# Kernel tuning notes

Measured on AMD Instinct MI355X. Metric: run time of the kernel, lower is better.

The kernel has to match this reference:

```python
import jax, jax.numpy as jnp
import numpy as np

SCALE = 1.0
P0 = 0.1


def setup_inputs() -> dict:
    key = jax.random.key(0)
    k1, k2, k3, k4 = jax.random.split(key, 4)
    B, N, D, T, TM = 64, 2048, 128, 512, 512
    data = jax.random.normal(k1, (B, N, D), dtype=jnp.float32)
    targets = jax.random.normal(k2, (B, N), dtype=jnp.float32)
    W = jax.random.normal(k3, (D, T), dtype=jnp.float32)        # major task pool, (n_dims, n_tasks)
    W_minor = jax.random.normal(k4, (D, TM), dtype=jnp.float32)  # minor task pool
    return {"data": data, "targets": targets, "W": W, "W_minor": W_minor}


def reference(data, targets, W, W_minor):
    # data: (B, N, D); targets: (B, N); W: (D, T); W_minor: (D, TM)
    n_minor = W_minor.shape[1]
    W_all = jnp.concatenate([W, W_minor], axis=1)            # (D, T_total)
    XW = jnp.einsum('bnd,dt->bnt', data, W_all)              # (B, N, T_total)
    diff2 = (targets[..., None] - XW) ** 2                   # (B, N, T_total)
    # Prefix sum-of-squared-residuals: step i uses points 0..i-1 (step 0 -> zeros,
    # matching the original's zeros-prefix call).
    prefix = jnp.cumsum(diff2, axis=1)
    prefix = jnp.concatenate([jnp.zeros_like(prefix[:, :1]), prefix[:, :-1]], axis=1)
    # Log priors: original hardcodes log((1-p0)/3) for major tasks (kept faithfully).
    log_prior_major = float(np.log((1.0 - P0) / 3.0))
    log_prior_minor = float(np.log(P0 / n_minor))
    log_prior = jnp.concatenate([
        jnp.full((W.shape[1],), log_prior_major, dtype=data.dtype),
        jnp.full((n_minor,), log_prior_minor, dtype=data.dtype),
    ])                                                        # (T_total,)
    log_probs = -0.5 * prefix / (SCALE ** 2) + log_prior      # (B, N, T_total)
    weights = jax.nn.softmax(log_probs, axis=-1)              # posterior over tasks
    w_mmse = jnp.einsum('bnt,dt->bnd', weights, W_all)        # (B, N, D)
    preds = jnp.sum(data * w_mmse, axis=-1)                   # (B, N)
    return preds
```

## Files before the change

kernel.cpp:

```cpp
#include <hip/hip_runtime.h>

typedef _Float16 half8 __attribute__((ext_vector_type(8)));
typedef float floatx4 __attribute__((ext_vector_type(4)));

#define NB 64
#define NN 2048
#define ND 128
#define NT 1024
#define NC 16
#define NCHUNKS 128
#define NIV 64

#define ALPHA 0.84932184f
#define INV_ALPHA 1.17741002f
#define LP2_MAJOR (-1.7369655941662063f)
#define LP2_MINOR (-12.321928094887362f)

__device__ __forceinline__ float fexp2(float x) {
  float r;
  asm("v_exp_f32 %0, %1" : "=v"(r) : "v"(x));
  return r;
}

#define PIN8(x) asm volatile("" : "+v"(x))

template <int CTRL>
__device__ __forceinline__ float dppshr_add(float x) {
  int i = __builtin_bit_cast(int, x);
  int s = __builtin_amdgcn_update_dpp(0, i, CTRL, 0xF, 0xF, true);
  return x + __builtin_bit_cast(float, s);
}
__device__ __forceinline__ float scan16(float x) {
  x = dppshr_add<0x111>(x);
  x = dppshr_add<0x112>(x);
  x = dppshr_add<0x114>(x);
  x = dppshr_add<0x118>(x);
  return x;
}
__device__ __forceinline__ float bcast15(float x) {
  int i = __builtin_bit_cast(int, x);
  i = __builtin_amdgcn_ds_swizzle(i, 0x1F0);
  return __builtin_bit_cast(float, i);
}

__global__ void k_prep(const float* __restrict__ W, const float* __restrict__ Wm,
                       _Float16* __restrict__ Wph, _Float16* __restrict__ Wpl) {
  int idx = blockIdx.x * 256 + threadIdx.x;
  int t = idx >> 7, d = idx & 127;
  float x = (t < 512) ? W[d * 512 + t] : Wm[d * 512 + (t - 512)];
  x *= ALPHA;
  _Float16 h = (_Float16)x;
  _Float16 l = (_Float16)(x - (float)h);
  Wph[idx] = h;
  Wpl[idx] = l;
}

__global__ void k_prep_data(const float* __restrict__ data,
                            _Float16* __restrict__ Apk) {
  int idx = blockIdx.x * 256 + threadIdx.x;
  int l = idx & 63, kk = (idx >> 6) & 3, ch = (idx >> 8) & 127, b = idx >> 15;
  int row = ch * 16 + (l & 15);
  int dcol = kk * 32 + (l >> 4) * 8;
  const float* src = data + ((size_t)b * NN + row) * ND + dcol;
  floatx4 a0 = *(const floatx4*)src;
  floatx4 a1 = *(const floatx4*)(src + 4);
  half8 h, lo;
#pragma unroll
  for (int j = 0; j < 4; ++j) {
    h[j] = (_Float16)a0[j];
    lo[j] = (_Float16)(a0[j] - (float)h[j]);
    h[4 + j] = (_Float16)a1[j];
    lo[4 + j] = (_Float16)(a1[j] - (float)h[4 + j]);
  }
  size_t o = ((size_t)(b * 128 + ch)) * 4096 + kk * 512 + l * 8;
  *(half8*)(Apk + o) = h;
  *(half8*)(Apk + o + 2048) = lo;
}

__global__ __launch_bounds__(512, 4)
void k_fused(const _Float16* __restrict__ Apk, const float* __restrict__ targets,
             const _Float16* __restrict__ Wph, const _Float16* __restrict__ Wpl,
             floatx4* __restrict__ part) {
  int bid = blockIdx.x;
  int xcd = bid & 7, rest = bid >> 3;
  int tq = rest & 7, b = (rest >> 3) * 8 + xcd;
  int tid = threadIdx.x;
  int w = tid >> 6, l = tid & 63;
  int l15 = l & 15, lhi = l >> 4;
  int wavebase = tq * 128 + w * 16;

  half8 wh[4], wl[4];
#pragma unroll
  for (int kk = 0; kk < 4; ++kk) {
    int off = (wavebase + l15) * 128 + kk * 32 + lhi * 8;
    wh[kk] = *(const half8*)(Wph + off);
    wl[kk] = *(const half8*)(Wpl + off);
  }
#pragma unroll
  for (int kk = 0; kk < 4; ++kk) { PIN8(wh[kk]); PIN8(wl[kk]); }

  float prior2 = (tq < 4) ? LP2_MAJOR : LP2_MINOR;
  float run[4] = {0.f, 0.f, 0.f, 0.f};

  const _Float16* abase = Apk + (size_t)b * 128 * 4096;
  const float* tgp = targets + (size_t)b * NN + l15;
  size_t pbase = (size_t)b * NN * 8 + tq;

  __shared__ _Float16 Abuf[2][2][4096];
  __shared__ float sm[8][4][65][3];

  int wslot = w * 512 + l * 8;

#define EPI(ACC, SLOT, TGOFF)                                         \
  do {                                                                \
    float tgs = tgp[TGOFF] * ALPHA;                                   \
    float q[4], inc[4], lp[4];                                        \
    _Pragma("unroll")                                                 \
    for (int r = 0; r < 4; ++r) {                                     \
      float d = tgs - ACC[r];                                         \
      q[r] = d * d;                                                   \
    }                                                                 \
    _Pragma("unroll")                                                 \
    for (int r = 0; r < 4; ++r) inc[r] = scan16(q[r]);                \
    _Pragma("unroll")                                                 \
    for (int r = 0; r < 4; ++r)                                       \
      lp[r] = (prior2 - run[r]) + (q[r] - inc[r]);                    \
    _Pragma("unroll")                                                 \
    for (int r = 0; r < 4; ++r) run[r] += bcast15(inc[r]);            \
    float m = fmaxf(fmaxf(lp[0], lp[1]), fmaxf(lp[2], lp[3]));        \
    float s1 = 0.f, s2 = 0.f;                                         \
    _Pragma("unroll")                                                 \
    for (int r = 0; r < 4; ++r) {                                     \
      float e = fexp2(lp[r] - m);                                     \
      s1 += e;                                                        \
      s2 = fmaf(e, ACC[r], s2);                                       \
    }                                                                 \
    sm[w][SLOT][l][0] = m;                                            \
    sm[w][SLOT][l][1] = s1;                                           \
    sm[w][SLOT][l][2] = s2;                                           \
  } while (0)

#define GEMM3(ACC, AH, AL)                                                        \
  do {                                                                            \
    floatx4 hh = {0.f, 0.f, 0.f, 0.f};                                            \
    floatx4 hl = {0.f, 0.f, 0.f, 0.f};                                            \
    floatx4 lh = {0.f, 0.f, 0.f, 0.f};                                            \
    _Pragma("unroll")                                                             \
    for (int kk = 0; kk < 4; ++kk) {                                              \
      hh = __builtin_amdgcn_mfma_f32_16x16x32_f16(wh[kk], AH[kk], hh, 0, 0, 0);   \
      hl = __builtin_amdgcn_mfma_f32_16x16x32_f16(wh[kk], AL[kk], hl, 0, 0, 0);   \
      lh = __builtin_amdgcn_mfma_f32_16x16x32_f16(wl[kk], AH[kk], lh, 0, 0, 0);   \
    }                                                                             \
    ACC = (hh + hl) + lh;                                                         \
  } while (0)

  half8 s0 = *(const half8*)(abase + wslot);
  half8 s1 = *(const half8*)(abase + 4096 + wslot);
  *(half8*)&Abuf[0][0][wslot] = s0;
  *(half8*)&Abuf[0][1][wslot] = s1;
  s0 = *(const half8*)(abase + 2 * 4096 + wslot);
  s1 = *(const half8*)(abase + 3 * 4096 + wslot);
  __syncthreads();

  for (int iv = 0; iv < NIV; ++iv) {
    int cur = iv & 1;
    half8 ahA[4], alA[4];
#pragma unroll
    for (int kk = 0; kk < 4; ++kk) {
      ahA[kk] = *(const half8*)&Abuf[cur][0][kk * 512 + l * 8];
      alA[kk] = *(const half8*)&Abuf[cur][0][2048 + kk * 512 + l * 8];
    }
    floatx4 accA;
    GEMM3(accA, ahA, alA);
    half8 ahB[4], alB[4];
#pragma unroll
    for (int kk = 0; kk < 4; ++kk) {
      ahB[kk] = *(const half8*)&Abuf[cur][1][kk * 512 + l * 8];
      alB[kk] = *(const half8*)&Abuf[cur][1][2048 + kk * 512 + l * 8];
    }
    floatx4 accB;
    GEMM3(accB, ahB, alB);

    *(half8*)&Abuf[cur ^ 1][0][wslot] = s0;
    *(half8*)&Abuf[cur ^ 1][1][wslot] = s1;
    int pfA = 2 * iv + 4, pfB = 2 * iv + 5;
    pfA = pfA > 127 ? 127 : pfA;
    pfB = pfB > 127 ? 127 : pfB;
    s0 = *(const half8*)(abase + (size_t)pfA * 4096 + wslot);
    s1 = *(const half8*)(abase + (size_t)pfB * 4096 + wslot);

    EPI(accA, ((2 * iv) & 3), 0);
    EPI(accB, ((2 * iv + 1) & 3), 16);

    if (iv & 1) {
      __syncthreads();
      if (tid < 64) {
        int c4 = tid >> 4, row = tid & 15;
        float M = -3.4e38f;
#pragma unroll
        for (int wv = 0; wv < 8; ++wv)
#pragma unroll
          for (int g = 0; g < 4; ++g)
            M = fmaxf(M, sm[wv][c4][g * 16 + row][0]);
        float S1 = 0.f, S2 = 0.f;
#pragma unroll
        for (int wv = 0; wv < 8; ++wv)
#pragma unroll
          for (int g = 0; g < 4; ++g) {
            float e = fexp2(sm[wv][c4][g * 16 + row][0] - M);
            S1 = fmaf(sm[wv][c4][g * 16 + row][1], e, S1);
            S2 = fmaf(sm[wv][c4][g * 16 + row][2], e, S2);
          }
        floatx4 v;
        v[0] = M; v[1] = S1; v[2] = S2; v[3] = 0.f;
        part[pbase + (size_t)((2 * iv - 2 + c4) * 16 + row) * 8] = v;
      }
    }
    __syncthreads();
    tgp += 32;
  }
#undef EPI
#undef GEMM3
}

__global__ void k_combine(const floatx4* __restrict__ part, float* __restrict__ out) {
  int idx = blockIdx.x * 256 + threadIdx.x;
  const floatx4* p = part + (size_t)idx * 8;
  floatx4 v[8];
  float M = -3.4e38f;
#pragma unroll
  for (int j = 0; j < 8; ++j) { v[j] = p[j]; M = fmaxf(M, v[j][0]); }
  float s1 = 0.f, s2 = 0.f;
#pragma unroll
  for (int j = 0; j < 8; ++j) {
    float e = fexp2(v[j][0] - M);
    s1 += v[j][1] * e;
    s2 += v[j][2] * e;
  }
  out[idx] = s2 / s1 * INV_ALPHA;
}

extern "C" void kernel_launch(void* const* d_in, const int* in_sizes, int n_in,
                              void* d_out, int out_size, void* d_ws, size_t ws_size,
                              hipStream_t stream) {
  const float* data    = (const float*)d_in[0];
  const float* targets = (const float*)d_in[1];
  const float* W       = (const float*)d_in[2];
  const float* Wm      = (const float*)d_in[3];
  float* out = (float*)d_out;

  char* ws = (char*)d_ws;
  const size_t MB = 1u << 20;
  _Float16* Wph  = (_Float16*)ws;
  _Float16* Wpl  = (_Float16*)(ws + 256 * 1024);
  _Float16* Apk  = (_Float16*)(ws + 512 * 1024);
  floatx4* part  = (floatx4*)(ws + 512 * 1024 + 64 * MB);

  k_prep<<<512, 256, 0, stream>>>(W, Wm, Wph, Wpl);
  k_prep_data<<<8192, 256, 0, stream>>>(data, Apk);
  k_fused<<<NB * 8, 512, 0, stream>>>(Apk, targets, Wph, Wpl, part);
  k_combine<<<(NB * NN) / 256, 256, 0, stream>>>(part, out);
}
```

Measured before the change: 182.3 us.

## Give each wave two task tiles and halve block size in fused kernel

Each wave now holds two 16-task weight tiles in registers and reuses every A fragment loaded from LDS for both tiles, so each block runs 4 waves of 256 threads instead of 8. This halves the LDS reads of A per MFMA and halves the softmax partial-merge work across waves. The cost is double the register footprint for the weights and accumulators and fewer waves per block, which may lower occupancy and latency hiding.

```diff
diff --git a/kernel.cpp b/kernel.cpp
--- a/kernel.cpp
+++ b/kernel.cpp
@@ -77,7 +77,7 @@
   *(half8*)(Apk + o + 2048) = lo;
 }
 
-__global__ __launch_bounds__(512, 4)
+__global__ __launch_bounds__(256, 2)
 void k_fused(const _Float16* __restrict__ Apk, const float* __restrict__ targets,
              const _Float16* __restrict__ Wph, const _Float16* __restrict__ Wpl,
              floatx4* __restrict__ part) {
@@ -87,110 +87,134 @@
   int tid = threadIdx.x;
   int w = tid >> 6, l = tid & 63;
   int l15 = l & 15, lhi = l >> 4;
-  int wavebase = tq * 128 + w * 16;
-
-  half8 wh[4], wl[4];
-#pragma unroll
-  for (int kk = 0; kk < 4; ++kk) {
-    int off = (wavebase + l15) * 128 + kk * 32 + lhi * 8;
-    wh[kk] = *(const half8*)(Wph + off);
-    wl[kk] = *(const half8*)(Wpl + off);
-  }
-#pragma unroll
-  for (int kk = 0; kk < 4; ++kk) { PIN8(wh[kk]); PIN8(wl[kk]); }
+  int wavebase = tq * 128 + w * 32;
+
+  half8 wh[2][4], wl[2][4];
+#pragma unroll
+  for (int tt = 0; tt < 2; ++tt)
+#pragma unroll
+    for (int kk = 0; kk < 4; ++kk) {
+      int off = (wavebase + tt * 16 + l15) * 128 + kk * 32 + lhi * 8;
+      wh[tt][kk] = *(const half8*)(Wph + off);
+      wl[tt][kk] = *(const half8*)(Wpl + off);
+    }
+#pragma unroll
+  for (int tt = 0; tt < 2; ++tt)
+#pragma unroll
+    for (int kk = 0; kk < 4; ++kk) { PIN8(wh[tt][kk]); PIN8(wl[tt][kk]); }
 
   float prior2 = (tq < 4) ? LP2_MAJOR : LP2_MINOR;
-  float run[4] = {0.f, 0.f, 0.f, 0.f};
+  float run[2][4] = {{0.f, 0.f, 0.f, 0.f}, {0.f, 0.f, 0.f, 0.f}};
 
   const _Float16* abase = Apk + (size_t)b * 128 * 4096;
   const float* tgp = targets + (size_t)b * NN + l15;
   size_t pbase = (size_t)b * NN * 8 + tq;
 
-  __shared__ _Float16 Abuf[2][2][4096];
-  __shared__ float sm[8][4][65][3];
-
-  int wslot = w * 512 + l * 8;
-
-#define EPI(ACC, SLOT, TGOFF)                                         \
+  __shared__ _Float16 Abuf[2][8192];
+  __shared__ float sm[4][4][65][3];
+
+  int t8 = tid * 8;
+
+#define GEMM3(ACC, TT, AH, AL)                                                      \
+  do {                                                                              \
+    floatx4 hh = {0.f, 0.f, 0.f, 0.f};                                              \
+    floatx4 hl = {0.f, 0.f, 0.f, 0.f};                                              \
+    floatx4 lh = {0.f, 0.f, 0.f, 0.f};                                              \
+    _Pragma("unroll")                                                               \
+    for (int kk = 0; kk < 4; ++kk) {                                                \
+      hh = __builtin_amdgcn_mfma_f32_16x16x32_f16(wh[TT][kk], AH[kk], hh, 0, 0, 0); \
+      hl = __builtin_amdgcn_mfma_f32_16x16x32_f16(wh[TT][kk], AL[kk], hl, 0, 0, 0); \
+      lh = __builtin_amdgcn_mfma_f32_16x16x32_f16(wl[TT][kk], AH[kk], lh, 0, 0, 0); \
+    }                                                                               \
+    ACC = (hh + hl) + lh;                                                           \
+  } while (0)
+
+#define EPI(ACC0, ACC1, SLOT, TGOFF)                                  \
   do {                                                                \
     float tgs = tgp[TGOFF] * ALPHA;                                   \
-    float q[4], inc[4], lp[4];                                        \
+    float q[2][4], inc[2][4], lp[2][4];                               \
     _Pragma("unroll")                                                 \
     for (int r = 0; r < 4; ++r) {                                     \
-      float d = tgs - ACC[r];                                         \
-      q[r] = d * d;                                                   \
+      float d0 = tgs - ACC0[r], d1 = tgs - ACC1[r];                   \
+      q[0][r] = d0 * d0; q[1][r] = d1 * d1;                           \
     }                                                                 \
     _Pragma("unroll")                                                 \
-    for (int r = 0; r < 4; ++r) inc[r] = scan16(q[r]);                \
-    _Pragma("unroll")                                                 \
-    for (int r = 0; r < 4; ++r)                                       \
-      lp[r] = (prior2 - run[r]) + (q[r] - inc[r]);                    \
-    _Pragma("unroll")                                                 \
-    for (int r = 0; r < 4; ++r) run[r] += bcast15(inc[r]);            \
-    float m = fmaxf(fmaxf(lp[0], lp[1]), fmaxf(lp[2], lp[3]));        \
+    for (int tt = 0; tt < 2; ++tt)                                    \
+      _Pragma("unroll")                                               \
+      for (int r = 0; r < 4; ++r) inc[tt][r] = scan16(q[tt][r]);      \
+    _Pragma("unroll")                                                 \
+    for (int tt = 0; tt < 2; ++tt)                                    \
+      _Pragma("unroll")                                               \
+      for (int r = 0; r < 4; ++r) {                                   \
+        lp[tt][r] = (prior2 - run[tt][r]) + (q[tt][r] - inc[tt][r]);  \
+        run[tt][r] += bcast15(inc[tt][r]);                            \
+      }                                                               \
+    float m = fmaxf(fmaxf(fmaxf(lp[0][0], lp[0][1]),                  \
+                          fmaxf(lp[0][2], lp[0][3])),                 \
+                    fmaxf(fmaxf(lp[1][0], lp[1][1]),                  \
+                          fmaxf(lp[1][2], lp[1][3])));                \
     float s1 = 0.f, s2 = 0.f;                                         \
     _Pragma("unroll")                                                 \
     for (int r = 0; r < 4; ++r) {                                     \
-      float e = fexp2(lp[r] - m);                                     \
-      s1 += e;                                                        \
-      s2 = fmaf(e, ACC[r], s2);                                       \
+      float e0 = fexp2(lp[0][r] - m), e1 = fexp2(lp[1][r] - m);       \
+      s1 += e0 + e1;                                                  \
+      s2 = fmaf(e0, ACC0[r], s2);                                     \
+      s2 = fmaf(e1, ACC1[r], s2);                                     \
     }                                                                 \
     sm[w][SLOT][l][0] = m;                                            \
     sm[w][SLOT][l][1] = s1;                                           \
     sm[w][SLOT][l][2] = s2;                                           \
   } while (0)
 
-#define GEMM3(ACC, AH, AL)                                                        \
-  do {                                                                            \
-    floatx4 hh = {0.f, 0.f, 0.f, 0.f};                                            \
-    floatx4 hl = {0.f, 0.f, 0.f, 0.f};                                            \
-    floatx4 lh = {0.f, 0.f, 0.f, 0.f};                                            \
-    _Pragma("unroll")                                                             \
-    for (int kk = 0; kk < 4; ++kk) {                                              \
-      hh = __builtin_amdgcn_mfma_f32_16x16x32_f16(wh[kk], AH[kk], hh, 0, 0, 0);   \
-      hl = __builtin_amdgcn_mfma_f32_16x16x32_f16(wh[kk], AL[kk], hl, 0, 0, 0);   \
-      lh = __builtin_amdgcn_mfma_f32_16x16x32_f16(wl[kk], AH[kk], lh, 0, 0, 0);   \
-    }                                                                             \
-    ACC = (hh + hl) + lh;                                                         \
-  } while (0)
-
-  half8 s0 = *(const half8*)(abase + wslot);
-  half8 s1 = *(const half8*)(abase + 4096 + wslot);
-  *(half8*)&Abuf[0][0][wslot] = s0;
-  *(half8*)&Abuf[0][1][wslot] = s1;
-  s0 = *(const half8*)(abase + 2 * 4096 + wslot);
-  s1 = *(const half8*)(abase + 3 * 4096 + wslot);
+  half8 s0 = *(const half8*)(abase + t8);
+  half8 s1_ = *(const half8*)(abase + 2048 + t8);
+  half8 s2_ = *(const half8*)(abase + 4096 + t8);
+  half8 s3 = *(const half8*)(abase + 6144 + t8);
+  *(half8*)&Abuf[0][t8] = s0;
+  *(half8*)&Abuf[0][2048 + t8] = s1_;
+  *(half8*)&Abuf[0][4096 + t8] = s2_;
+  *(half8*)&Abuf[0][6144 + t8] = s3;
+  s0 = *(const half8*)(abase + 8192 + t8);
+  s1_ = *(const half8*)(abase + 8192 + 2048 + t8);
+  s2_ = *(const half8*)(abase + 8192 + 4096 + t8);
+  s3 = *(const half8*)(abase + 8192 + 6144 + t8);
   __syncthreads();
 
   for (int iv = 0; iv < NIV; ++iv) {
     int cur = iv & 1;
-    half8 ahA[4], alA[4];
+    half8 ah[4], al[4];
 #pragma unroll
     for (int kk = 0; kk < 4; ++kk) {
-      ahA[kk] = *(const half8*)&Abuf[cur][0][kk * 512 + l * 8];
-      alA[kk] = *(const half8*)&Abuf[cur][0][2048 + kk * 512 + l * 8];
-    }
-    floatx4 accA;
-    GEMM3(accA, ahA, alA);
-    half8 ahB[4], alB[4];
+      ah[kk] = *(const half8*)&Abuf[cur][kk * 512 + l * 8];
+      al[kk] = *(const half8*)&Abuf[cur][2048 + kk * 512 + l * 8];
+    }
+    floatx4 accA0, accA1;
+    GEMM3(accA0, 0, ah, al);
+    GEMM3(accA1, 1, ah, al);
 #pragma unroll
     for (int kk = 0; kk < 4; ++kk) {
-      ahB[kk] = *(const half8*)&Abuf[cur][1][kk * 512 + l * 8];
-      alB[kk] = *(const half8*)&Abuf[cur][1][2048 + kk * 512 + l * 8];
-    }
-    floatx4 accB;
-    GEMM3(accB, ahB, alB);
-
-    *(half8*)&Abuf[cur ^ 1][0][wslot] = s0;
-    *(half8*)&Abuf[cur ^ 1][1][wslot] = s1;
-    int pfA = 2 * iv + 4, pfB = 2 * iv + 5;
-    pfA = pfA > 127 ? 127 : pfA;
-    pfB = pfB > 127 ? 127 : pfB;
-    s0 = *(const half8*)(abase + (size_t)pfA * 4096 + wslot);
-    s1 = *(const half8*)(abase + (size_t)pfB * 4096 + wslot);
-
-    EPI(accA, ((2 * iv) & 3), 0);
-    EPI(accB, ((2 * iv + 1) & 3), 16);
+      ah[kk] = *(const half8*)&Abuf[cur][4096 + kk * 512 + l * 8];
+      al[kk] = *(const half8*)&Abuf[cur][6144 + kk * 512 + l * 8];
+    }
+    floatx4 accB0, accB1;
+    GEMM3(accB0, 0, ah, al);
+    GEMM3(accB1, 1, ah, al);
+
+    *(half8*)&Abuf[cur ^ 1][t8] = s0;
+    *(half8*)&Abuf[cur ^ 1][2048 + t8] = s1_;
+    *(half8*)&Abuf[cur ^ 1][4096 + t8] = s2_;
+    *(half8*)&Abuf[cur ^ 1][6144 + t8] = s3;
+    {
+      int pf = iv + 2 > 63 ? 63 : iv + 2;
+      const _Float16* pp = abase + (size_t)pf * 8192 + t8;
+      s0 = *(const half8*)pp;
+      s1_ = *(const half8*)(pp + 2048);
+      s2_ = *(const half8*)(pp + 4096);
+      s3 = *(const half8*)(pp + 6144);
+    }
+
+    EPI(accA0, accA1, ((2 * iv) & 3), 0);
+    EPI(accB0, accB1, ((2 * iv + 1) & 3), 16);
 
     if (iv & 1) {
       __syncthreads();
@@ -198,13 +222,13 @@
         int c4 = tid >> 4, row = tid & 15;
         float M = -3.4e38f;
 #pragma unroll
-        for (int wv = 0; wv < 8; ++wv)
+        for (int wv = 0; wv < 4; ++wv)
 #pragma unroll
           for (int g = 0; g < 4; ++g)
             M = fmaxf(M, sm[wv][c4][g * 16 + row][0]);
         float S1 = 0.f, S2 = 0.f;
 #pragma unroll
-        for (int wv = 0; wv < 8; ++wv)
+        for (int wv = 0; wv < 4; ++wv)
 #pragma unroll
           for (int g = 0; g < 4; ++g) {
             float e = fexp2(sm[wv][c4][g * 16 + row][0] - M);
@@ -258,6 +282,6 @@
 
   k_prep<<<512, 256, 0, stream>>>(W, Wm, Wph, Wpl);
   k_prep_data<<<8192, 256, 0, stream>>>(data, Apk);
-  k_fused<<<NB * 8, 512, 0, stream>>>(Apk, targets, Wph, Wpl, part);
+  k_fused<<<NB * 8, 256, 0, stream>>>(Apk, targets, Wph, Wpl, part);
   k_combine<<<(NB * NN) / 256, 256, 0, stream>>>(part, out);
 }
```

Measured after the change: 176.8 us. 1.03x faster.
